# Optimization experiments

Measured on AMD Instinct MI355X. Metric: run time of the kernel, lower is better.

## Reference

```python
import jax, jax.numpy as jnp
import numpy as np

NUM_ENT = 50000
N = 4 * NUM_ENT          # concat of id/gender/age/level embeds along dim 0
D = 128                  # init_dim = gcn_dim = embed_dim
H = 4                    # k_kernel attention heads
E = 600000
NUM_REL = 10
B = 4096


def _seg_softmax(scores, seg, n):
    # scores: [E, H], softmax over edges sharing the same destination node
    m = jax.ops.segment_max(scores, seg, num_segments=n)
    m = jnp.where(jnp.isfinite(m), m, 0.0)
    e = jnp.exp(scores - m[seg])
    s = jax.ops.segment_sum(e, seg, num_segments=n)
    return e / (s[seg] + 1e-16)


def _rgat_conv(x, rel_emb, src, dst, edge_type, W, W_rel, att):
    # CompGCN-style relational message (x_src + r_et) @ W, GAT-style attention,
    # per-destination segment softmax, scatter-sum aggregate, tanh activation.
    n = x.shape[0]
    xW = x @ W                        # [N, D_out]
    rW = rel_emb @ W                  # relation embed in message space
    d_out = xW.shape[1]
    dh = d_out // H
    m = (xW[src] + rW[edge_type]).reshape(-1, H, dh)   # [E, H, dh] messages
    q = xW[dst].reshape(-1, H, dh)                     # [E, H, dh] dest feats
    score = jax.nn.leaky_relu(
        (q * att[:, :dh]).sum(-1) + (m * att[:, dh:]).sum(-1), 0.2)  # [E, H]
    alpha = _seg_softmax(score, dst, n)                # [E, H]
    out = jax.ops.segment_sum((alpha[..., None] * m).reshape(-1, d_out), dst,
                              num_segments=n)          # [N, D_out]
    return jnp.tanh(out), rel_emb @ W_rel


def setup_inputs() -> dict:
    key = jax.random.key(0)
    ks = jax.random.split(key, 16)
    s = 0.1  # weight scale for numerical sanity
    return {
        "sub": jax.random.randint(ks[0], (B,), 0, N),
        "rel": jax.random.randint(ks[1], (B,), 0, 2 * NUM_REL),
        "edge_index": jax.random.randint(ks[2], (2, E), 0, N),
        "edge_type": jax.random.randint(ks[3], (E,), 0, 2 * NUM_REL),
        "ent_feature": jax.random.randint(ks[4], (NUM_ENT, 3), 0, 8),
        "gender_weight": s * jax.random.normal(ks[5], (8, D), jnp.float32),
        "age_weight": s * jax.random.normal(ks[6], (8, D), jnp.float32),
        "level_weight": s * jax.random.normal(ks[7], (8, D), jnp.float32),
        "id_embed": s * jax.random.normal(ks[8], (NUM_ENT, D), jnp.float32),
        "init_rel": s * jax.random.normal(ks[9], (2 * NUM_REL, D), jnp.float32),
        "W1": s * jax.random.normal(ks[10], (D, D), jnp.float32),
        "Wr1": s * jax.random.normal(ks[11], (D, D), jnp.float32),
        "att1": s * jax.random.normal(ks[12], (H, 2 * (D // H)), jnp.float32),
        "W2": s * jax.random.normal(ks[13], (D, D), jnp.float32),
        "Wr2": s * jax.random.normal(ks[14], (D, D), jnp.float32),
        "att2": s * jax.random.normal(ks[15], (H, 2 * (D // H)), jnp.float32),
    }


def reference(sub, rel, edge_index, edge_type, ent_feature,
              gender_weight, age_weight, level_weight, id_embed, init_rel,
              W1, Wr1, att1, W2, Wr2, att2):
    # feature embedding gathers + concat along node axis (as in __init__)
    gender_embed = gender_weight[ent_feature[:, 0]]
    age_embed = age_weight[ent_feature[:, 1]]
    level_embed = level_weight[ent_feature[:, 2]]
    x = jnp.concatenate([id_embed, gender_embed, age_embed, level_embed], axis=0)  # [N, D]
    src, dst = edge_index[0], edge_index[1]
    r = init_rel
    x, r = _rgat_conv(x, r, src, dst, edge_type, W1, Wr1, att1)
    # dropout modules run as identity (eval mode)
    x, r = _rgat_conv(x, r, src, dst, edge_type, W2, Wr2, att2)
    sub_emb = x[sub]
    rel_emb = r[rel]
    return (sub_emb, rel_emb, x)
```

## Files before the change

### kernel.cpp

```cpp
#include <hip/hip_runtime.h>

#define D 128
#define HEADS 4

typedef __attribute__((ext_vector_type(8))) short short8;
typedef __attribute__((ext_vector_type(4))) short s16x4;
typedef __attribute__((ext_vector_type(4))) float f32x4;

__device__ __forceinline__ short f2b(float f) {
    unsigned u = __float_as_uint(f);
    unsigned r = (u + 0x7FFFu + ((u >> 16) & 1u)) >> 16;
    return (short)r;
}

__device__ __forceinline__ float fast_tanh(float x) {
    float e = __expf(2.0f * x);
    return 1.0f - 2.0f / (e + 1.0f);
}

__global__ __launch_bounds__(256) void gemm_mfma(
    const unsigned short* __restrict__ Ab, const short* __restrict__ Wt,
    unsigned short* __restrict__ C, const float* __restrict__ att,
    float* __restrict__ ns, int buildmode, long Mrows,
    const int* __restrict__ ent_feature, const float* __restrict__ gw,
    const float* __restrict__ aw, const float* __restrict__ lw,
    const float* __restrict__ idemb, int num_ent)
{
    __shared__ short sA[64 * D];
    __shared__ short sW[D * D];
    __shared__ float attL[256];

    const int t = threadIdx.x;

    #pragma unroll
    for (int i = 0; i < 8; ++i) {
        int c = t + 256 * i;
        int row = c >> 4, kb = c & 15;
        short8 blk = *(const short8*)(Wt + c * 8);
        *(short8*)&sW[row * D + (kb ^ (row & 7)) * 8] = blk;
    }
    attL[t] = att[t];

    for (int sub = 0; sub < 2; ++sub) {
        const long row0 = (long)blockIdx.x * 128 + sub * 64;
        if (row0 >= Mrows) break;
        if (sub) __syncthreads();

        {
            int srow = t >> 2;
            int q = t & 3;
            long grow = row0 + srow;
            if (buildmode == 2) {
                const short8* p8 = (const short8*)(Ab + grow * D);
                #pragma unroll
                for (int jb = 0; jb < 4; ++jb) {
                    short8 blk = p8[q * 4 + jb];
                    int kb = (q * 4 + jb) ^ (srow & 7);
                    *(short8*)&sA[srow * D + kb * 8] = blk;
                }
            } else {
                const float* srcp;
                if (grow < num_ent)               srcp = idemb + grow * D;
                else if (grow < 2L * num_ent)     srcp = gw + (long)ent_feature[(grow - num_ent) * 3 + 0] * D;
                else if (grow < 3L * num_ent)     srcp = aw + (long)ent_feature[(grow - 2L * num_ent) * 3 + 1] * D;
                else                              srcp = lw + (long)ent_feature[(grow - 3L * num_ent) * 3 + 2] * D;
                const float4* p4 = (const float4*)srcp + q * 8;
                float v[32];
                #pragma unroll
                for (int j = 0; j < 8; ++j) {
                    float4 f = p4[j];
                    v[j * 4 + 0] = f.x; v[j * 4 + 1] = f.y; v[j * 4 + 2] = f.z; v[j * 4 + 3] = f.w;
                }
                #pragma unroll
                for (int jb = 0; jb < 4; ++jb) {
                    short8 blk;
                    #pragma unroll
                    for (int e = 0; e < 8; ++e) blk[e] = f2b(v[jb * 8 + e]);
                    int kb = (q * 4 + jb) ^ (srow & 7);
                    *(short8*)&sA[srow * D + kb * 8] = blk;
                }
            }
        }
        __syncthreads();

        const int wv = t >> 6, lane = t & 63;
        const int cl = lane & 15, kg = lane >> 4;

        short8 a[4];
        #pragma unroll
        for (int ks = 0; ks < 4; ++ks)
            a[ks] = *(const short8*)&sA[(wv * 16 + cl) * D + (((ks * 4 + kg) ^ (cl & 7)) * 8)];

        f32x4 acc[8];
        #pragma unroll
        for (int ct = 0; ct < 8; ++ct) acc[ct] = (f32x4){0.f, 0.f, 0.f, 0.f};

        #pragma unroll
        for (int ct = 0; ct < 8; ++ct) {
            #pragma unroll
            for (int ks = 0; ks < 4; ++ks) {
                short8 b = *(const short8*)&sW[(ct * 16 + cl) * D + (((ks * 4 + kg) ^ (cl & 7)) * 8)];
                acc[ct] = __builtin_amdgcn_mfma_f32_16x16x32_bf16(b, a[ks], acc[ct], 0, 0, 0);
            }
        }

        {
            unsigned short* Crow = C + (row0 + wv * 16 + cl) * D + kg * 4;
            #pragma unroll
            for (int ct = 0; ct < 8; ++ct) {
                s16x4 v;
                #pragma unroll
                for (int j = 0; j < 4; ++j) v[j] = f2b(acc[ct][j]);
                *(s16x4*)(Crow + ct * 16) = v;
            }
        }

        {
            float qp[4] = {0.f, 0.f, 0.f, 0.f};
            float sp[4] = {0.f, 0.f, 0.f, 0.f};
            #pragma unroll
            for (int ct = 0; ct < 8; ++ct) {
                int h = ct >> 1;
                int base = h * 64 + (ct & 1) * 16 + kg * 4;
                f32x4 aq4 = *(const f32x4*)&attL[base];
                f32x4 am4 = *(const f32x4*)&attL[base + 32];
                #pragma unroll
                for (int j = 0; j < 4; ++j) {
                    qp[h] = fmaf(acc[ct][j], aq4[j], qp[h]);
                    sp[h] = fmaf(acc[ct][j], am4[j], sp[h]);
                }
            }
            #pragma unroll
            for (int h = 0; h < 4; ++h) {
                qp[h] += __shfl_xor(qp[h], 16);
                qp[h] += __shfl_xor(qp[h], 32);
                sp[h] += __shfl_xor(sp[h], 16);
                sp[h] += __shfl_xor(sp[h], 32);
            }
            float qv = qp[0], sv = sp[0];
            if (kg == 1) { qv = qp[1]; sv = sp[1]; }
            else if (kg == 2) { qv = qp[2]; sv = sp[2]; }
            else if (kg == 3) { qv = qp[3]; sv = sp[3]; }
            long rown = row0 + wv * 16 + cl;
            ns[rown * 8 + kg] = qv;
            ns[rown * 8 + 4 + kg] = sv;
        }
    }
}

__global__ void prep1(const float* __restrict__ init_rel,
                      const float* __restrict__ W1, const float* __restrict__ Wr1,
                      const float* __restrict__ W2, const float* __restrict__ att1,
                      unsigned short* __restrict__ rw16, float* __restrict__ r1,
                      float* __restrict__ srt,
                      short* __restrict__ Wt1, short* __restrict__ Wt2, int nrel)
{
    __shared__ float red[128];
    int b = blockIdx.x, c = threadIdx.x;
    if (b >= 2 * nrel) {
        int bb = b - 2 * nrel;
        const float* W = (bb < D) ? W1 : W2;
        short* Wt = (bb < D) ? Wt1 : Wt2;
        int n = bb & (D - 1);
        Wt[n * D + c] = f2b(W[c * D + n]);
        return;
    }
    int r = (b < nrel) ? b : b - nrel;
    const float* W = (b < nrel) ? W1 : Wr1;
    float s = 0.f;
    for (int k = 0; k < D; ++k) s = fmaf(init_rel[r * D + k], W[k * D + c], s);
    if (b < nrel) {
        rw16[r * D + c] = (unsigned short)f2b(s);
        int h = c >> 5;
        red[c] = s * att1[h * 64 + 32 + (c & 31)];
        __syncthreads();
        if (c < 4) {
            float ss = 0.f;
            #pragma unroll
            for (int k = 0; k < 32; ++k) ss += red[c * 32 + k];
            srt[r * 4 + c] = ss;
        }
    } else {
        r1[r * D + c] = s;
    }
}

__global__ void prep2(const float* __restrict__ r1,
                      const float* __restrict__ W2, const float* __restrict__ Wr2,
                      const float* __restrict__ att2,
                      unsigned short* __restrict__ rw16, float* __restrict__ r2,
                      float* __restrict__ srt, int nrel)
{
    __shared__ float red[128];
    int b = blockIdx.x, c = threadIdx.x;
    int r = (b < nrel) ? b : b - nrel;
    const float* W = (b < nrel) ? W2 : Wr2;
    float s = 0.f;
    for (int k = 0; k < D; ++k) s = fmaf(r1[r * D + k], W[k * D + c], s);
    if (b < nrel) {
        rw16[r * D + c] = (unsigned short)f2b(s);
        int h = c >> 5;
        red[c] = s * att2[h * 64 + 32 + (c & 31)];
        __syncthreads();
        if (c < 4) {
            float ss = 0.f;
            #pragma unroll
            for (int k = 0; k < 32; ++k) ss += red[c * 32 + k];
            srt[r * 4 + c] = ss;
        }
    } else {
        r2[r * D + c] = s;
    }
}

__global__ __launch_bounds__(256) void hist_deg(const int* __restrict__ dst,
                                                int* __restrict__ deg, int E_)
{
    int i = blockIdx.x * 256 + threadIdx.x;
    if (i < E_) atomicAdd(&deg[dst[i]], 1);
}

__global__ __launch_bounds__(256) void scan_local(const int* __restrict__ deg,
                                                  int* __restrict__ offs,
                                                  int* __restrict__ partial, int n)
{
    __shared__ int lds[256];
    int b = blockIdx.x, t = threadIdx.x;
    int base = b * 1024;
    int v[4]; int s = 0;
    #pragma unroll
    for (int j = 0; j < 4; ++j) {
        int idx = base + t * 4 + j;
        v[j] = idx < n ? deg[idx] : 0;
        s += v[j];
    }
    lds[t] = s;
    __syncthreads();
    int mysum = s;
    for (int off = 1; off < 256; off <<= 1) {
        int o = t >= off ? lds[t - off] : 0;
        __syncthreads();
        lds[t] += o;
        __syncthreads();
    }
    int excl = lds[t] - mysum;
    if (t == 255) partial[b] = lds[255];
    int run = excl;
    #pragma unroll
    for (int j = 0; j < 4; ++j) {
        int idx = base + t * 4 + j;
        if (idx < n) offs[idx] = run;
        run += v[j];
    }
}

__global__ void scan_partials(int* __restrict__ partial, int nb,
                              int* __restrict__ offs, int n)
{
    __shared__ int lds[256];
    int t = threadIdx.x;
    int v = (t < nb) ? partial[t] : 0;
    lds[t] = v;
    __syncthreads();
    int my = v;
    for (int off = 1; off < 256; off <<= 1) {
        int o = (t >= off) ? lds[t - off] : 0;
        __syncthreads();
        lds[t] += o;
        __syncthreads();
    }
    if (t < nb) partial[t] = lds[t] - my;
    if (t == 255) offs[n] = lds[255];
}

__global__ __launch_bounds__(256) void scan_add(int* __restrict__ offs,
                                                const int* __restrict__ partial, int n)
{
    int idx = blockIdx.x * 256 + threadIdx.x;
    if (idx < n) offs[idx] += partial[idx >> 10];
}

__global__ __launch_bounds__(256) void scatter_edges(
    const int* __restrict__ src, const int* __restrict__ dst, const int* __restrict__ etype,
    const int* __restrict__ offs, int* __restrict__ deg,
    unsigned* __restrict__ sorted, int E_)
{
    int i = blockIdx.x * 256 + threadIdx.x;
    if (i >= E_) return;
    int d = dst[i];
    int pos = offs[d] + atomicSub(&deg[d], 1) - 1;
    sorted[pos] = ((unsigned)src[i] << 8) | (unsigned)etype[i];
}

#define GATHER_SLOT(mb, sv, rv, sr, p, cond)                                 \
    unsigned mb = 0, rv = 0; float sv = 0.f, sr = 0.f;                       \
    if (cond) { unsigned rowb = (p) & 0xFFFFFF00u;                           \
        unsigned etb = ((p) & 0xFFu) << 8;                                   \
        mb = *(const unsigned*)(xb + rowb + lo4);                            \
        sv = *(const float*)(nb + (rowb >> 3) + ho4);                        \
        rv = *(const unsigned*)(rb + etb + lo4);                             \
        sr = *(const float*)(sb + (etb >> 4) + (ho4 - 16)); }

#define ACCUM_SLOT(mb, sv, rv, sr, cond)                                     \
    if (cond) {                                                              \
        float mx = __uint_as_float(mb << 16) + __uint_as_float(rv << 16);    \
        float my = __uint_as_float(mb & 0xFFFF0000u) + __uint_as_float(rv & 0xFFFF0000u); \
        float sc = qd + sv + sr; sc = sc > 0.f ? sc : 0.2f * sc;             \
        float we = __expf(sc);                                               \
        srun += we; ax = fmaf(we, mx, ax); ay = fmaf(we, my, ay); }

__global__ __launch_bounds__(256) void agg_node(
    const int* __restrict__ offs, const unsigned* __restrict__ sedge,
    const unsigned short* __restrict__ xWb, const unsigned short* __restrict__ rw16,
    const float* __restrict__ ns, const float* __restrict__ srt,
    void* __restrict__ outx, int out_bf16, int Nn)
{
    int wid = threadIdx.x >> 6;
    int lane = threadIdx.x & 63;
    long node = (long)blockIdx.x * 4 + wid;
    if (node >= Nn) return;
    int h = lane >> 4;

    const char* xb = (const char*)xWb;
    const char* rb = (const char*)rw16;
    const char* nb = (const char*)ns;
    const char* sb = (const char*)srt;
    const int lo4 = 4 * lane;
    const int ho4 = 16 + 4 * h;

    float qd = ns[node * 8 + h];
    int e0 = offs[node], e1 = offs[node + 1];
    float srun = 0.f, ax = 0.f, ay = 0.f;

    for (int base = e0; base < e1; base += 4) {
        unsigned p0 = sedge[base];
        unsigned p1 = (base + 1 < e1) ? sedge[base + 1] : 0;
        unsigned p2 = (base + 2 < e1) ? sedge[base + 2] : 0;
        unsigned p3 = (base + 3 < e1) ? sedge[base + 3] : 0;

        GATHER_SLOT(m0, v0, r0, s0, p0, true)
        GATHER_SLOT(m1, v1, r1, s1, p1, base + 1 < e1)
        GATHER_SLOT(m2, v2, r2, s2, p2, base + 2 < e1)
        GATHER_SLOT(m3, v3, r3, s3, p3, base + 3 < e1)

        ACCUM_SLOT(m0, v0, r0, s0, true)
        ACCUM_SLOT(m1, v1, r1, s1, base + 1 < e1)
        ACCUM_SLOT(m2, v2, r2, s2, base + 2 < e1)
        ACCUM_SLOT(m3, v3, r3, s3, base + 3 < e1)
    }

    float inv = 1.0f / (srun + 1e-16f);
    float ox = fast_tanh(ax * inv);
    float oy = fast_tanh(ay * inv);
    if (out_bf16) {
        unsigned pk = ((unsigned)(unsigned short)f2b(oy) << 16) | (unsigned short)f2b(ox);
        *(unsigned*)((unsigned short*)outx + node * D + 2 * lane) = pk;
    } else {
        float2 o; o.x = ox; o.y = oy;
        *(float2*)((float*)outx + node * D + 2 * lane) = o;
    }
}

__global__ void gather_out(const int* __restrict__ sub, const int* __restrict__ rel,
                           const float* __restrict__ xsrc, const float* __restrict__ rsrc,
                           float* __restrict__ out_sub, float* __restrict__ out_rel, int b)
{
    long i = (long)blockIdx.x * 256 + threadIdx.x;
    long tot = (long)b * 32;
    if (i < tot) {
        long row = i >> 5; int q = (int)(i & 31);
        ((float4*)out_sub)[i] = ((const float4*)(xsrc + (long)sub[row] * D))[q];
    } else if (i < 2 * tot) {
        long j = i - tot;
        long row = j >> 5; int q = (int)(j & 31);
        ((float4*)out_rel)[j] = ((const float4*)(rsrc + (long)rel[row] * D))[q];
    }
}

extern "C" void kernel_launch(void* const* d_in, const int* in_sizes, int n_in,
                              void* d_out, int out_size, void* d_ws, size_t ws_size,
                              hipStream_t stream)
{
    const int*   sub        = (const int*)d_in[0];
    const int*   rel        = (const int*)d_in[1];
    const int*   edge_index = (const int*)d_in[2];
    const int*   edge_type  = (const int*)d_in[3];
    const int*   ent_feat   = (const int*)d_in[4];
    const float* gw         = (const float*)d_in[5];
    const float* aw         = (const float*)d_in[6];
    const float* lw         = (const float*)d_in[7];
    const float* idemb      = (const float*)d_in[8];
    const float* init_rel   = (const float*)d_in[9];
    const float* W1         = (const float*)d_in[10];
    const float* Wr1        = (const float*)d_in[11];
    const float* att1       = (const float*)d_in[12];
    const float* W2         = (const float*)d_in[13];
    const float* Wr2        = (const float*)d_in[14];
    const float* att2       = (const float*)d_in[15];

    const int  Bn      = in_sizes[0];
    const int  E_      = in_sizes[3];
    const int  num_ent = in_sizes[4] / 3;
    const long Nn      = 4L * num_ent;
    const int  nrel    = in_sizes[9] / D;

    const int* srcp = edge_index;
    const int* dstp = edge_index + E_;

    float* out_sub = (float*)d_out;
    float* out_rel = out_sub + (long)Bn * D;
    float* out_x   = out_rel + (long)Bn * D;

    unsigned short* xWb = (unsigned short*)d_ws;
    unsigned short* x1b = xWb + Nn * D;
    int*      offs   = (int*)(x1b + Nn * D);
    int*      deg    = offs + (Nn + 4);
    unsigned* sorted = (unsigned*)(deg + Nn);
    int*      partial= (int*)(sorted + E_);
    unsigned short* rw16 = (unsigned short*)(partial + 1024);
    float* r1     = (float*)(rw16 + (long)nrel * D);
    float* r2     = r1 + (long)nrel * D;
    short* Wt1    = (short*)(r2 + (long)nrel * D);
    short* Wt2    = Wt1 + D * D;
    float* ns     = (float*)(Wt2 + D * D);
    float* srt    = ns + Nn * 8;

    dim3 blk(256);
    int gemm_blocks  = (int)((Nn + 127) / 128);
    int e_blocks     = (E_ + 255) / 256;
    int agg_blocks   = (int)((Nn + 3) / 4);
    int gat_blocks   = (int)((2L * Bn * 32 + 255) / 256);
    int scan_blocks  = (int)((Nn + 1023) / 1024);
    int sadd_blocks  = (int)((Nn + 255) / 256);

    prep1<<<2 * nrel + 256, D, 0, stream>>>(init_rel, W1, Wr1, W2, att1,
                                            rw16, r1, srt, Wt1, Wt2, nrel);

    hipMemsetAsync(deg, 0, Nn * sizeof(int), stream);
    hist_deg<<<e_blocks, blk, 0, stream>>>(dstp, deg, E_);
    scan_local<<<scan_blocks, blk, 0, stream>>>(deg, offs, partial, (int)Nn);
    scan_partials<<<1, 256, 0, stream>>>(partial, scan_blocks, offs, (int)Nn);
    scan_add<<<sadd_blocks, blk, 0, stream>>>(offs, partial, (int)Nn);
    scatter_edges<<<e_blocks, blk, 0, stream>>>(srcp, dstp, edge_type, offs, deg, sorted, E_);

    gemm_mfma<<<gemm_blocks, blk, 0, stream>>>(nullptr, Wt1, xWb, att1, ns, 1, Nn,
                                               ent_feat, gw, aw, lw, idemb, num_ent);
    agg_node<<<agg_blocks, blk, 0, stream>>>(offs, sorted, xWb, rw16, ns, srt, x1b, 1, (int)Nn);

    prep2<<<2 * nrel, D, 0, stream>>>(r1, W2, Wr2, att2, rw16, r2, srt, nrel);
    gemm_mfma<<<gemm_blocks, blk, 0, stream>>>(x1b, Wt2, xWb, att2, ns, 2, Nn,
                                               nullptr, nullptr, nullptr, nullptr, nullptr, num_ent);
    agg_node<<<agg_blocks, blk, 0, stream>>>(offs, sorted, xWb, rw16, ns, srt, out_x, 0, (int)Nn);

    gather_out<<<gat_blocks, blk, 0, stream>>>(sub, rel, out_x, r2, out_sub, out_rel, Bn);
}
```

Before: 282.9 us.

## Precompute per-edge attention exp weights in a separate edge-parallel kernel

Adds an edge_we kernel that computes the leaky-relu-exp attention weight for every sorted edge and all four heads once, using a new per-edge destination array written during the scatter. agg_node then reads one precomputed float per edge and head instead of gathering source and relation score terms and evaluating exp on every lane. This removes the redundant per-lane exp and the scattered score loads from the aggregation loop. In exchange it adds a kernel launch per layer, an extra E-sized int array and a 16-byte-per-edge weight buffer that has to be written and then read back.

```diff
diff --git a/kernel.cpp b/kernel.cpp
--- a/kernel.cpp
+++ b/kernel.cpp
@@ -283,36 +283,58 @@
 __global__ __launch_bounds__(256) void scatter_edges(
     const int* __restrict__ src, const int* __restrict__ dst, const int* __restrict__ etype,
     const int* __restrict__ offs, int* __restrict__ deg,
-    unsigned* __restrict__ sorted, int E_)
+    unsigned* __restrict__ sorted, int* __restrict__ sortedD, int E_)
 {
     int i = blockIdx.x * 256 + threadIdx.x;
     if (i >= E_) return;
     int d = dst[i];
     int pos = offs[d] + atomicSub(&deg[d], 1) - 1;
     sorted[pos] = ((unsigned)src[i] << 8) | (unsigned)etype[i];
-}
-
-#define GATHER_SLOT(mb, sv, rv, sr, p, cond)                                 \
-    unsigned mb = 0, rv = 0; float sv = 0.f, sr = 0.f;                       \
+    sortedD[pos] = d;
+}
+
+__global__ __launch_bounds__(256) void edge_we(
+    const unsigned* __restrict__ sorted, const int* __restrict__ sortedD,
+    const float* __restrict__ ns, const float* __restrict__ srt,
+    float* __restrict__ we, int E_)
+{
+    int i = blockIdx.x * 256 + threadIdx.x;
+    if (i >= E_) return;
+    unsigned p = sorted[i];
+    int d = sortedD[i];
+    int s = (int)(p >> 8);
+    int et = (int)(p & 0xFFu);
+    f32x4 qd = *(const f32x4*)(ns + (long)d * 8);
+    f32x4 sm = *(const f32x4*)(ns + (long)s * 8 + 4);
+    f32x4 sr = *(const f32x4*)(srt + et * 4);
+    f32x4 o;
+    #pragma unroll
+    for (int h = 0; h < 4; ++h) {
+        float sc = qd[h] + sm[h] + sr[h];
+        sc = sc > 0.f ? sc : 0.2f * sc;
+        o[h] = __expf(sc);
+    }
+    *(f32x4*)(we + (long)i * 4) = o;
+}
+
+#define GATHER_SLOT(mb, rv, wv_, p, i_, cond)                                \
+    unsigned mb = 0, rv = 0; float wv_ = 0.f;                                \
     if (cond) { unsigned rowb = (p) & 0xFFFFFF00u;                           \
         unsigned etb = ((p) & 0xFFu) << 8;                                   \
         mb = *(const unsigned*)(xb + rowb + lo4);                            \
-        sv = *(const float*)(nb + (rowb >> 3) + ho4);                        \
         rv = *(const unsigned*)(rb + etb + lo4);                             \
-        sr = *(const float*)(sb + (etb >> 4) + (ho4 - 16)); }
-
-#define ACCUM_SLOT(mb, sv, rv, sr, cond)                                     \
+        wv_ = *(const float*)(wb + ((long)(i_) << 4) + h4); }
+
+#define ACCUM_SLOT(mb, rv, wv_, cond)                                        \
     if (cond) {                                                              \
         float mx = __uint_as_float(mb << 16) + __uint_as_float(rv << 16);    \
         float my = __uint_as_float(mb & 0xFFFF0000u) + __uint_as_float(rv & 0xFFFF0000u); \
-        float sc = qd + sv + sr; sc = sc > 0.f ? sc : 0.2f * sc;             \
-        float we = __expf(sc);                                               \
-        srun += we; ax = fmaf(we, mx, ax); ay = fmaf(we, my, ay); }
+        srun += wv_; ax = fmaf(wv_, mx, ax); ay = fmaf(wv_, my, ay); }
 
 __global__ __launch_bounds__(256) void agg_node(
     const int* __restrict__ offs, const unsigned* __restrict__ sedge,
     const unsigned short* __restrict__ xWb, const unsigned short* __restrict__ rw16,
-    const float* __restrict__ ns, const float* __restrict__ srt,
+    const float* __restrict__ we,
     void* __restrict__ outx, int out_bf16, int Nn)
 {
     int wid = threadIdx.x >> 6;
@@ -323,12 +345,10 @@
 
     const char* xb = (const char*)xWb;
     const char* rb = (const char*)rw16;
-    const char* nb = (const char*)ns;
-    const char* sb = (const char*)srt;
+    const char* wb = (const char*)we;
     const int lo4 = 4 * lane;
-    const int ho4 = 16 + 4 * h;
-
-    float qd = ns[node * 8 + h];
+    const int h4 = 4 * h;
+
     int e0 = offs[node], e1 = offs[node + 1];
     float srun = 0.f, ax = 0.f, ay = 0.f;
 
@@ -338,15 +358,15 @@
         unsigned p2 = (base + 2 < e1) ? sedge[base + 2] : 0;
         unsigned p3 = (base + 3 < e1) ? sedge[base + 3] : 0;
 
-        GATHER_SLOT(m0, v0, r0, s0, p0, true)
-        GATHER_SLOT(m1, v1, r1, s1, p1, base + 1 < e1)
-        GATHER_SLOT(m2, v2, r2, s2, p2, base + 2 < e1)
-        GATHER_SLOT(m3, v3, r3, s3, p3, base + 3 < e1)
-
-        ACCUM_SLOT(m0, v0, r0, s0, true)
-        ACCUM_SLOT(m1, v1, r1, s1, base + 1 < e1)
-        ACCUM_SLOT(m2, v2, r2, s2, base + 2 < e1)
-        ACCUM_SLOT(m3, v3, r3, s3, base + 3 < e1)
+        GATHER_SLOT(m0, r0, w0, p0, base, true)
+        GATHER_SLOT(m1, r1, w1, p1, base + 1, base + 1 < e1)
+        GATHER_SLOT(m2, r2, w2, p2, base + 2, base + 2 < e1)
+        GATHER_SLOT(m3, r3, w3, p3, base + 3, base + 3 < e1)
+
+        ACCUM_SLOT(m0, r0, w0, true)
+        ACCUM_SLOT(m1, r1, w1, base + 1 < e1)
+        ACCUM_SLOT(m2, r2, w2, base + 2 < e1)
+        ACCUM_SLOT(m3, r3, w3, base + 3 < e1)
     }
 
     float inv = 1.0f / (srun + 1e-16f);
@@ -416,7 +436,8 @@
     int*      offs   = (int*)(x1b + Nn * D);
     int*      deg    = offs + (Nn + 4);
     unsigned* sorted = (unsigned*)(deg + Nn);
-    int*      partial= (int*)(sorted + E_);
+    int*      sortedD= (int*)(sorted + E_);
+    int*      partial= sortedD + E_;
     unsigned short* rw16 = (unsigned short*)(partial + 1024);
     float* r1     = (float*)(rw16 + (long)nrel * D);
     float* r2     = r1 + (long)nrel * D;
@@ -424,6 +445,7 @@
     short* Wt2    = Wt1 + D * D;
     float* ns     = (float*)(Wt2 + D * D);
     float* srt    = ns + Nn * 8;
+    float* web    = srt + (long)nrel * HEADS;
 
     dim3 blk(256);
     int gemm_blocks  = (int)((Nn + 127) / 128);
@@ -441,16 +463,19 @@
     scan_local<<<scan_blocks, blk, 0, stream>>>(deg, offs, partial, (int)Nn);
     scan_partials<<<1, 256, 0, stream>>>(partial, scan_blocks, offs, (int)Nn);
     scan_add<<<sadd_blocks, blk, 0, stream>>>(offs, partial, (int)Nn);
-    scatter_edges<<<e_blocks, blk, 0, stream>>>(srcp, dstp, edge_type, offs, deg, sorted, E_);
+    scatter_edges<<<e_blocks, blk, 0, stream>>>(srcp, dstp, edge_type, offs, deg,
+                                                sorted, sortedD, E_);
 
     gemm_mfma<<<gemm_blocks, blk, 0, stream>>>(nullptr, Wt1, xWb, att1, ns, 1, Nn,
                                                ent_feat, gw, aw, lw, idemb, num_ent);
-    agg_node<<<agg_blocks, blk, 0, stream>>>(offs, sorted, xWb, rw16, ns, srt, x1b, 1, (int)Nn);
+    edge_we<<<e_blocks, blk, 0, stream>>>(sorted, sortedD, ns, srt, web, E_);
+    agg_node<<<agg_blocks, blk, 0, stream>>>(offs, sorted, xWb, rw16, web, x1b, 1, (int)Nn);
 
     prep2<<<2 * nrel, D, 0, stream>>>(r1, W2, Wr2, att2, rw16, r2, srt, nrel);
     gemm_mfma<<<gemm_blocks, blk, 0, stream>>>(x1b, Wt2, xWb, att2, ns, 2, Nn,
                                                nullptr, nullptr, nullptr, nullptr, nullptr, num_ent);
-    agg_node<<<agg_blocks, blk, 0, stream>>>(offs, sorted, xWb, rw16, ns, srt, out_x, 0, (int)Nn);
+    edge_we<<<e_blocks, blk, 0, stream>>>(sorted, sortedD, ns, srt, web, E_);
+    agg_node<<<agg_blocks, blk, 0, stream>>>(offs, sorted, xWb, rw16, web, out_x, 0, (int)Nn);
 
     gather_out<<<gat_blocks, blk, 0, stream>>>(sub, rel, out_x, r2, out_sub, out_rel, Bn);
 }
```

Result: no change. 287.8 us (+1.7%).

## Fuse CSR build into one cooperative kernel and make aggregation grid-stride

Applied to the files above, without the earlier changes.

The memset, degree histogram, three-stage scan and edge scatter are merged into a single cooperative kernel that separates the phases with grid-wide syncs. This removes several launches and the gaps between them. The aggregation kernel now runs a fixed 2048-block grid that loops over nodes with a stride instead of launching one wave per node. The trade-off is the cost of grid.sync, a grid limited to 196 blocks for the edge passes, and the tail balance of the persistent aggregation loop.

```diff
diff --git a/kernel.cpp b/kernel.cpp
--- a/kernel.cpp
+++ b/kernel.cpp
@@ -1,4 +1,7 @@
 #include <hip/hip_runtime.h>
+#include <hip/hip_cooperative_groups.h>
+
+namespace cg = cooperative_groups;
 
 #define D 128
 #define HEADS 4
@@ -213,83 +216,81 @@
     }
 }
 
-__global__ __launch_bounds__(256) void hist_deg(const int* __restrict__ dst,
-                                                int* __restrict__ deg, int E_)
-{
-    int i = blockIdx.x * 256 + threadIdx.x;
-    if (i < E_) atomicAdd(&deg[dst[i]], 1);
-}
-
-__global__ __launch_bounds__(256) void scan_local(const int* __restrict__ deg,
-                                                  int* __restrict__ offs,
-                                                  int* __restrict__ partial, int n)
-{
+__global__ __launch_bounds__(256) void csr_build(
+    const int* __restrict__ src, const int* __restrict__ dst,
+    const int* __restrict__ etype,
+    int* __restrict__ deg, int* __restrict__ offs, int* __restrict__ partial,
+    unsigned* __restrict__ sorted, int n, int E_)
+{
+    cg::grid_group grid = cg::this_grid();
     __shared__ int lds[256];
-    int b = blockIdx.x, t = threadIdx.x;
-    int base = b * 1024;
-    int v[4]; int s = 0;
-    #pragma unroll
-    for (int j = 0; j < 4; ++j) {
-        int idx = base + t * 4 + j;
-        v[j] = idx < n ? deg[idx] : 0;
-        s += v[j];
-    }
-    lds[t] = s;
-    __syncthreads();
-    int mysum = s;
-    for (int off = 1; off < 256; off <<= 1) {
-        int o = t >= off ? lds[t - off] : 0;
-        __syncthreads();
-        lds[t] += o;
-        __syncthreads();
-    }
-    int excl = lds[t] - mysum;
-    if (t == 255) partial[b] = lds[255];
-    int run = excl;
-    #pragma unroll
-    for (int j = 0; j < 4; ++j) {
-        int idx = base + t * 4 + j;
-        if (idx < n) offs[idx] = run;
-        run += v[j];
-    }
-}
-
-__global__ void scan_partials(int* __restrict__ partial, int nb,
-                              int* __restrict__ offs, int n)
-{
-    __shared__ int lds[256];
-    int t = threadIdx.x;
-    int v = (t < nb) ? partial[t] : 0;
-    lds[t] = v;
-    __syncthreads();
-    int my = v;
-    for (int off = 1; off < 256; off <<= 1) {
-        int o = (t >= off) ? lds[t - off] : 0;
-        __syncthreads();
-        lds[t] += o;
-        __syncthreads();
-    }
-    if (t < nb) partial[t] = lds[t] - my;
-    if (t == 255) offs[n] = lds[255];
-}
-
-__global__ __launch_bounds__(256) void scan_add(int* __restrict__ offs,
-                                                const int* __restrict__ partial, int n)
-{
-    int idx = blockIdx.x * 256 + threadIdx.x;
-    if (idx < n) offs[idx] += partial[idx >> 10];
-}
-
-__global__ __launch_bounds__(256) void scatter_edges(
-    const int* __restrict__ src, const int* __restrict__ dst, const int* __restrict__ etype,
-    const int* __restrict__ offs, int* __restrict__ deg,
-    unsigned* __restrict__ sorted, int E_)
-{
-    int i = blockIdx.x * 256 + threadIdx.x;
-    if (i >= E_) return;
-    int d = dst[i];
-    int pos = offs[d] + atomicSub(&deg[d], 1) - 1;
-    sorted[pos] = ((unsigned)src[i] << 8) | (unsigned)etype[i];
+    const int tid = blockIdx.x * 256 + threadIdx.x;
+    const int nthreads = gridDim.x * 256;
+
+    for (int i = tid; i < n; i += nthreads) deg[i] = 0;
+    grid.sync();
+
+    for (int i = tid; i < E_; i += nthreads) atomicAdd(&deg[dst[i]], 1);
+    grid.sync();
+
+    {
+        int b = blockIdx.x, t = threadIdx.x;
+        int base = b * 1024;
+        int v[4]; int s = 0;
+        #pragma unroll
+        for (int j = 0; j < 4; ++j) {
+            int idx = base + t * 4 + j;
+            v[j] = idx < n ? deg[idx] : 0;
+            s += v[j];
+        }
+        lds[t] = s;
+        __syncthreads();
+        int mysum = s;
+        for (int off = 1; off < 256; off <<= 1) {
+            int o = t >= off ? lds[t - off] : 0;
+            __syncthreads();
+            lds[t] += o;
+            __syncthreads();
+        }
+        int excl = lds[t] - mysum;
+        if (t == 255) partial[b] = lds[255];
+        int run = excl;
+        #pragma unroll
+        for (int j = 0; j < 4; ++j) {
+            int idx = base + t * 4 + j;
+            if (idx < n) offs[idx] = run;
+            run += v[j];
+        }
+    }
+    grid.sync();
+
+    if (blockIdx.x == 0) {
+        int t = threadIdx.x;
+        int nb = gridDim.x;
+        int v = (t < nb) ? partial[t] : 0;
+        __syncthreads();
+        lds[t] = v;
+        __syncthreads();
+        int my = v;
+        for (int off = 1; off < 256; off <<= 1) {
+            int o = (t >= off) ? lds[t - off] : 0;
+            __syncthreads();
+            lds[t] += o;
+            __syncthreads();
+        }
+        if (t < nb) partial[t] = lds[t] - my;
+        if (t == 255) offs[n] = lds[255];
+    }
+    grid.sync();
+
+    for (int i = tid; i < n; i += nthreads) offs[i] += partial[i >> 10];
+    grid.sync();
+
+    for (int i = tid; i < E_; i += nthreads) {
+        int d = dst[i];
+        int pos = offs[d] + atomicSub(&deg[d], 1) - 1;
+        sorted[pos] = ((unsigned)src[i] << 8) | (unsigned)etype[i];
+    }
 }
 
 #define GATHER_SLOT(mb, sv, rv, sr, p, cond)                                 \
@@ -317,8 +318,6 @@
 {
     int wid = threadIdx.x >> 6;
     int lane = threadIdx.x & 63;
-    long node = (long)blockIdx.x * 4 + wid;
-    if (node >= Nn) return;
     int h = lane >> 4;
 
     const char* xb = (const char*)xWb;
@@ -328,36 +327,39 @@
     const int lo4 = 4 * lane;
     const int ho4 = 16 + 4 * h;
 
-    float qd = ns[node * 8 + h];
-    int e0 = offs[node], e1 = offs[node + 1];
-    float srun = 0.f, ax = 0.f, ay = 0.f;
-
-    for (int base = e0; base < e1; base += 4) {
-        unsigned p0 = sedge[base];
-        unsigned p1 = (base + 1 < e1) ? sedge[base + 1] : 0;
-        unsigned p2 = (base + 2 < e1) ? sedge[base + 2] : 0;
-        unsigned p3 = (base + 3 < e1) ? sedge[base + 3] : 0;
-
-        GATHER_SLOT(m0, v0, r0, s0, p0, true)
-        GATHER_SLOT(m1, v1, r1, s1, p1, base + 1 < e1)
-        GATHER_SLOT(m2, v2, r2, s2, p2, base + 2 < e1)
-        GATHER_SLOT(m3, v3, r3, s3, p3, base + 3 < e1)
-
-        ACCUM_SLOT(m0, v0, r0, s0, true)
-        ACCUM_SLOT(m1, v1, r1, s1, base + 1 < e1)
-        ACCUM_SLOT(m2, v2, r2, s2, base + 2 < e1)
-        ACCUM_SLOT(m3, v3, r3, s3, base + 3 < e1)
-    }
-
-    float inv = 1.0f / (srun + 1e-16f);
-    float ox = fast_tanh(ax * inv);
-    float oy = fast_tanh(ay * inv);
-    if (out_bf16) {
-        unsigned pk = ((unsigned)(unsigned short)f2b(oy) << 16) | (unsigned short)f2b(ox);
-        *(unsigned*)((unsigned short*)outx + node * D + 2 * lane) = pk;
-    } else {
-        float2 o; o.x = ox; o.y = oy;
-        *(float2*)((float*)outx + node * D + 2 * lane) = o;
+    const long wstride = (long)gridDim.x * 4;
+    for (long node = (long)blockIdx.x * 4 + wid; node < Nn; node += wstride) {
+        float qd = ns[node * 8 + h];
+        int e0 = offs[node], e1 = offs[node + 1];
+        float srun = 0.f, ax = 0.f, ay = 0.f;
+
+        for (int base = e0; base < e1; base += 4) {
+            unsigned p0 = sedge[base];
+            unsigned p1 = (base + 1 < e1) ? sedge[base + 1] : 0;
+            unsigned p2 = (base + 2 < e1) ? sedge[base + 2] : 0;
+            unsigned p3 = (base + 3 < e1) ? sedge[base + 3] : 0;
+
+            GATHER_SLOT(m0, v0, r0, s0, p0, true)
+            GATHER_SLOT(m1, v1, r1, s1, p1, base + 1 < e1)
+            GATHER_SLOT(m2, v2, r2, s2, p2, base + 2 < e1)
+            GATHER_SLOT(m3, v3, r3, s3, p3, base + 3 < e1)
+
+            ACCUM_SLOT(m0, v0, r0, s0, true)
+            ACCUM_SLOT(m1, v1, r1, s1, base + 1 < e1)
+            ACCUM_SLOT(m2, v2, r2, s2, base + 2 < e1)
+            ACCUM_SLOT(m3, v3, r3, s3, base + 3 < e1)
+        }
+
+        float inv = 1.0f / (srun + 1e-16f);
+        float ox = fast_tanh(ax * inv);
+        float oy = fast_tanh(ay * inv);
+        if (out_bf16) {
+            unsigned pk = ((unsigned)(unsigned short)f2b(oy) << 16) | (unsigned short)f2b(ox);
+            *(unsigned*)((unsigned short*)outx + node * D + 2 * lane) = pk;
+        } else {
+            float2 o; o.x = ox; o.y = oy;
+            *(float2*)((float*)outx + node * D + 2 * lane) = o;
+        }
     }
 }
 
@@ -427,21 +429,21 @@
 
     dim3 blk(256);
     int gemm_blocks  = (int)((Nn + 127) / 128);
-    int e_blocks     = (E_ + 255) / 256;
-    int agg_blocks   = (int)((Nn + 3) / 4);
+    int agg_blocks   = 2048;
     int gat_blocks   = (int)((2L * Bn * 32 + 255) / 256);
-    int scan_blocks  = (int)((Nn + 1023) / 1024);
-    int sadd_blocks  = (int)((Nn + 255) / 256);
+    int csr_blocks   = (int)((Nn + 1023) / 1024);
 
     prep1<<<2 * nrel + 256, D, 0, stream>>>(init_rel, W1, Wr1, W2, att1,
                                             rw16, r1, srt, Wt1, Wt2, nrel);
 
-    hipMemsetAsync(deg, 0, Nn * sizeof(int), stream);
-    hist_deg<<<e_blocks, blk, 0, stream>>>(dstp, deg, E_);
-    scan_local<<<scan_blocks, blk, 0, stream>>>(deg, offs, partial, (int)Nn);
-    scan_partials<<<1, 256, 0, stream>>>(partial, scan_blocks, offs, (int)Nn);
-    scan_add<<<sadd_blocks, blk, 0, stream>>>(offs, partial, (int)Nn);
-    scatter_edges<<<e_blocks, blk, 0, stream>>>(srcp, dstp, edge_type, offs, deg, sorted, E_);
+    {
+        int n_i = (int)Nn, e_i = E_;
+        void* args[] = { (void*)&srcp, (void*)&dstp, (void*)&edge_type,
+                         (void*)&deg, (void*)&offs, (void*)&partial,
+                         (void*)&sorted, (void*)&n_i, (void*)&e_i };
+        hipLaunchCooperativeKernel((void*)csr_build, dim3(csr_blocks), blk,
+                                   args, 0, stream);
+    }
 
     gemm_mfma<<<gemm_blocks, blk, 0, stream>>>(nullptr, Wt1, xWb, att1, ns, 1, Nn,
                                                ent_feat, gw, aw, lw, idemb, num_ent);
```

Measured after the change: 388.3 us. 1.37x slower.
